# Performance work log

Hardware: AMD Instinct MI355X
Metric: run time of the kernel (lower is better)

The kernel has to match this reference:

```python
import jax, jax.numpy as jnp
import numpy as np

IMG_W, IMG_H, STRIDE = 640, 360, 32
S = 72
FMAP_H, FMAP_W = IMG_H // STRIDE, IMG_W // STRIDE  # 11, 20
C_IN, C_AF = 512, 64
B, T = 8, 4
LEFT = [72., 60., 49., 39., 30., 22.]
RIGHT = [108., 120., 131., 141., 150., 158.]
BOTTOM = [165., 150., 141., 131., 120., 108., 100., 90., 80., 72., 60., 49., 39., 30., 15.]


def _side_anchors(angles, nb, ys, x=None, y=None):
    # replicates LaneATT generate_side_anchors / generate_anchor, vectorized
    if x is not None:
        sx = np.full(nb, x, np.float64); sy = np.linspace(1., 0., nb)
    else:
        sx = np.linspace(1., 0., nb); sy = np.full(nb, y, np.float64)
    t = np.tan(np.deg2rad(np.asarray(angles, np.float64)))  # [J]
    # xs[i,j,s] = (sx_i + (1 - ys_s - 1 + sy_i)/tan(angle_j)) * img_w
    xs = (sx[:, None, None] + (1. - ys[None, None, :] - 1. + sy[:, None, None]) / t[None, :, None]) * IMG_W
    n = nb * len(angles)
    A = np.zeros((n, 5 + len(ys)), np.float32)
    A[:, 2] = np.repeat(1. - sy, len(angles))
    A[:, 3] = np.repeat(sx, len(angles))
    A[:, 5:] = xs.reshape(n, len(ys)).astype(np.float32)
    return A


def _gen_anchors(ys):
    left = _side_anchors(LEFT, 72, ys, x=0.)
    right = _side_anchors(RIGHT, 72, ys, x=1.)
    bottom = _side_anchors(BOTTOM, 128, ys, y=1.)
    return np.concatenate([left, bottom, right], axis=0)


def setup_inputs() -> dict:
    key = jax.random.key(0)
    ks = jax.random.split(key, 10)
    anchors = _gen_anchors(np.linspace(1., 0., S))            # [A, 77]
    anchors_cut = _gen_anchors(np.linspace(1., 0., FMAP_H))   # [A, 16]
    A = anchors.shape[0]  # 2784
    # compute_anchor_cut_indices
    unclamped = np.flip(np.round(anchors_cut[:, 5:] / STRIDE), axis=1).astype(np.int32)  # [A, H]
    cut_xs = np.clip(unclamped, 0, FMAP_W - 1)
    invalid_mask = (unclamped < 0) | (unclamped > FMAP_W)
    D = C_AF * FMAP_H  # 704
    head_in = (T + 1) * D  # (time_window_size+1)*anchor_feat_channels*fmap_h = 3520
    inp = {
        'x': jax.random.normal(ks[0], (B, T, C_IN, FMAP_H, FMAP_W), jnp.float32),
        'conv1_w': jax.random.normal(ks[1], (C_AF, C_IN), jnp.float32) * 0.02,
        'conv1_b': jnp.zeros((C_AF,), jnp.float32),
        'att_w': jax.random.normal(ks[2], (D, A - 1), jnp.float32) * 0.001,
        'att_b': jnp.zeros((A - 1,), jnp.float32),
        'cls_w': jax.random.normal(ks[3], (head_in, 2), jnp.float32) * 0.001,
        'cls_b': jnp.zeros((2,), jnp.float32),
        'reg_w': jax.random.normal(ks[4], (head_in, S + 2), jnp.float32) * 0.001,
        'reg_b': jnp.zeros((S + 2,), jnp.float32),
        'anchors': jnp.asarray(anchors),
        'cut_xs': jnp.asarray(cut_xs),
        'invalid_mask': jnp.asarray(invalid_mask),
    }
    return inp


def reference(x, conv1_w, conv1_b, att_w, att_b, cls_w, cls_b, reg_w, reg_b,
              anchors, cut_xs, invalid_mask):
    B_, T_, _, H, W = x.shape
    A = anchors.shape[0]
    # conv1: 1x1 conv over backbone features
    feats = jnp.einsum('btchw,oc->btohw', x, conv1_w) + conv1_b[None, None, :, None, None]
    # cut_anchor_features: gather rois[b,t,c,a,h] = feats[b,t,c,h,cut_xs[a,h]]
    Hy = jnp.broadcast_to(jnp.arange(H), cut_xs.shape)       # [A, H]
    rois = feats[:, :, :, Hy, cut_xs]                        # [B, T, C_af, A, H]
    rois = jnp.where(invalid_mask[None, None, None], 0.0, rois)
    rois = jnp.transpose(rois, (0, 1, 3, 2, 4))              # [B, T, A, C_af, H]
    C_af = rois.shape[3]
    D = C_af * H
    past = rois[:, :-1].reshape(B_, T_ - 1, A, D)            # [B, T-1, A, D]
    cur = rois[:, -1].reshape(B_, A, D)                      # [B, A, D]
    # attention_mechanism: softmax scores scattered into off-diagonal of [A, A]
    scores = cur.reshape(B_ * A, D) @ att_w + att_b          # [B*A, A-1]
    att = jax.nn.softmax(scores, axis=1).reshape(B_, A, A - 1)
    j = jnp.arange(A)
    i = j[:, None]
    # column j of row i maps to source index j - (j>i); diagonal is zero
    k = jnp.minimum(jnp.where(j[None, :] > i, j[None, :] - 1, j[None, :]), A - 2)
    Ibd = jnp.broadcast_to(i, (A, A))
    M = jnp.where(jnp.eye(A, dtype=bool)[None], 0.0, att[:, Ibd, k])  # [B, A, A]
    att_feat = jnp.einsum('bia,bad->bid', M, cur)            # [B, A, D]
    # head input: [past frames | attention features | current frame]
    past_p = jnp.transpose(past, (0, 2, 1, 3)).reshape(B_ * A, (T_ - 1) * D)
    head_in = jnp.concatenate([past_p, att_feat.reshape(B_ * A, D), cur.reshape(B_ * A, D)], axis=1)
    cls = (head_in @ cls_w + cls_b).reshape(B_, A, 2)
    reg = (head_in @ reg_w + reg_b).reshape(B_, A, -1)       # [B, A, n_offsets+2]
    base = jnp.broadcast_to(anchors[None], (B_, A, anchors.shape[1]))
    # reg_proposals: [:, :, :2]=cls ; [:, :, 2] from anchor ; [:, :, 3:] = anchor + reg
    reg_proposals = jnp.concatenate([cls, base[..., 2:3], base[..., 3:] + reg], axis=-1)
    return reg_proposals  # [B, A, 5 + n_offsets]
```

## Files before the change

### kernel.cpp

```cpp
#include <hip/hip_runtime.h>

#define BB 8
#define TT 4
#define CIN 512
#define CAF 64
#define HH 11
#define WW 20
#define PP 220
#define PPAD 256
#define AREAL 2784
#define AP 2816
#define DD 704
#define NH 80
#define NHP 128
#define KH 3520
#define NATT 2783

typedef __attribute__((ext_vector_type(8))) short bf16x8;
typedef __attribute__((ext_vector_type(4))) float floatx4;

__device__ __forceinline__ short f2bf(float f) {
  unsigned u = __float_as_uint(f);
  u += 0x7fffu + ((u >> 16) & 1u);
  return (short)(u >> 16);
}
__device__ __forceinline__ float bf2f(short s) {
  return __uint_as_float(((unsigned)(unsigned short)s) << 16);
}

__device__ __forceinline__ void gload_lds16(const void* g, void* l) {
  __builtin_amdgcn_global_load_lds(
      (const __attribute__((address_space(1))) void*)g,
      (__attribute__((address_space(3))) void*)l, 16, 0, 0);
}

__global__ __launch_bounds__(256)
void transpose_x_kernel(const float* __restrict__ x, short* __restrict__ xT)
{
  int bt = blockIdx.x;
  int c0 = blockIdx.y * 32;
  __shared__ float xs[32 * PP];
  int tid = threadIdx.x;
  const float* xp = x + ((long)bt * CIN + c0) * PP;
  for (int i = tid; i < 32 * PP; i += 256) xs[i] = xp[i];
  __syncthreads();
  short* op = xT + (long)bt * PPAD * CIN + c0;
  for (int j = tid; j < PPAD * 32; j += 256) {
    int p = j >> 5, cc = j & 31;
    short v = 0;
    if (p < PP) v = f2bf(xs[cc * PP + p]);
    op[(long)p * CIN + cc] = v;
  }
}

__global__ void prep_wbf_kernel(const float* __restrict__ w, short* __restrict__ wb)
{
  int idx = blockIdx.x * 256 + threadIdx.x;
  if (idx >= 128 * CIN) return;
  int n = idx >> 9, c = idx & 511;
  wb[idx] = (n < CAF) ? f2bf(w[(long)n * CIN + c]) : (short)0;
}

__global__ void prep_gidx_kernel(const int* __restrict__ cut_xs, const int* __restrict__ invalid,
                                 int* __restrict__ gidx)
{
  int idx = blockIdx.x * 256 + threadIdx.x;
  if (idx >= AREAL * HH) return;
  int hh = idx % HH;
  gidx[idx] = invalid[idx] ? -1 : (hh * WW + cut_xs[idx]) * 128;
}

__global__ __launch_bounds__(256)
void gather_cur_kernel(const short* __restrict__ fpo_base, const int* __restrict__ gidx,
                       short* __restrict__ curR)
{
  int g = blockIdx.y;
  int idx = blockIdx.x * 256 + threadIdx.x;
  int a = idx / 88;
  int ch = idx - a * 88;
  int d0 = ch * 8;
  bf16x8 v = {};
  if (a < AREAL) {
    const short* fp = fpo_base + ((long)g * TT + 3) * PPAD * 128;
    #pragma unroll
    for (int e = 0; e < 8; ++e) {
      int d = d0 + e;
      int o = d / 11;
      int hh = d - o * 11;
      int gi = gidx[a * 11 + hh];
      v[e] = (gi < 0) ? (short)0 : fp[gi + o];
    }
  }
  *(bf16x8*)(curR + ((long)g * AP + a) * DD + d0) = v;
}

__global__ __launch_bounds__(256)
void gather_past_kernel(const short* __restrict__ fpo_base, const int* __restrict__ gidx,
                        short* __restrict__ pastR)
{
  int ty = blockIdx.y;
  int g = ty / 3, t = ty - g * 3;
  int idx = blockIdx.x * 256 + threadIdx.x;
  int a = idx / 88;
  int ch = idx - a * 88;
  int d0 = ch * 8;
  bf16x8 v = {};
  if (a < AREAL) {
    const short* fp = fpo_base + ((long)g * TT + t) * PPAD * 128;
    #pragma unroll
    for (int e = 0; e < 8; ++e) {
      int d = d0 + e;
      int o = d / 11;
      int hh = d - o * 11;
      int gi = gidx[a * 11 + hh];
      v[e] = (gi < 0) ? (short)0 : fp[gi + o];
    }
  }
  *(bf16x8*)(pastR + ((long)ty * AP + a) * DD + d0) = v;
}

__global__ __launch_bounds__(256)
void prep_attw_kernel(const float* __restrict__ att_w, short* __restrict__ attwT)
{
  int n0 = blockIdx.x * 32;
  int d0 = blockIdx.y * 32;
  __shared__ float tile[32][33];
  int tid = threadIdx.x;
  for (int i = tid; i < 1024; i += 256) {
    int r = i >> 5, c = i & 31;
    int d = d0 + r, n = n0 + c;
    tile[r][c] = (d < DD && n < NATT) ? att_w[(long)d * NATT + n] : 0.f;
  }
  __syncthreads();
  for (int i = tid; i < 1024; i += 256) {
    int r = i >> 5, c = i & 31;
    attwT[(long)(n0 + r) * DD + d0 + c] = f2bf(tile[c][r]);
  }
}

__global__ void prep_headw_kernel(const float* __restrict__ cls_w, const float* __restrict__ reg_w,
                                  short* __restrict__ headwT)
{
  long idx = (long)blockIdx.x * 256 + threadIdx.x;
  if (idx >= (long)NHP * KH) return;
  int n = (int)(idx / KH), k = (int)(idx % KH);
  float v = 0.f;
  if (n < 2) v = cls_w[(long)k * 2 + n];
  else if (n < 76) v = reg_w[(long)k * 74 + (n - 2)];
  headwT[idx] = f2bf(v);
}

__global__ __launch_bounds__(512, 2)
void gemm256_nt_kernel(const short* __restrict__ A, long long aBatch, int lda,
                       const short* __restrict__ Bt, long long bBatch, int ldb,
                       short* __restrict__ C, long long cBatch, int ldc,
                       int K, const float* __restrict__ bias, int biasN)
{
  int gx = gridDim.x, gy = gridDim.y;
  int nwg = gx * gy * gridDim.z;
  int o = blockIdx.x + gx * (blockIdx.y + gy * blockIdx.z);
  int xcd = o & 7, pos = o >> 3;
  int q = nwg >> 3, r = nwg & 7;
  int nid = (xcd < r ? xcd * (q + 1) : r * (q + 1) + (xcd - r) * q) + pos;
  int bx = nid % gx; int tq = nid / gx; int by = tq % gy; int bz = tq / gy;

  A  += (long long)bz * aBatch;
  Bt += (long long)bz * bBatch;
  C  += (long long)bz * cBatch;
  int M0 = by * 256, N0 = bx * 256;

  __shared__ short lds_a[2 * 256 * 64];
  __shared__ short lds_b[2 * 256 * 64];

  int tid = threadIdx.x, lane = tid & 63, w = tid >> 6;
  int wr = w >> 2, wc = w & 3;

  floatx4 acc[8][4];
  #pragma unroll
  for (int m = 0; m < 8; ++m)
    #pragma unroll
    for (int n = 0; n < 4; ++n) acc[m][n] = floatx4{0.f, 0.f, 0.f, 0.f};

  int rl = tid >> 3, sl = tid & 7;
  int ssl = sl ^ (rl & 7);
  const short* aS = A  + (long)(M0 + rl) * lda + ssl * 8;
  const short* bS = Bt + (long)(N0 + rl) * ldb + ssl * 8;
  char* la0 = (char*)lds_a;
  char* lb0 = (char*)lds_b;
  int wub = (tid & ~63) * 16;

  auto stage = [&](int kt, int buf) {
    long ko = (long)kt * 64;
    #pragma unroll
    for (int c = 0; c < 4; ++c) {
      gload_lds16(aS + (long)c * 64 * lda + ko, la0 + buf * 32768 + c * 8192 + wub);
      gload_lds16(bS + (long)c * 64 * ldb + ko, lb0 + buf * 32768 + c * 8192 + wub);
    }
  };
  auto rdA = [&](int buf, int mf, int kk) -> bf16x8 {
    int row = wr * 128 + mf * 16 + (lane & 15);
    int phys = (kk * 4 + (lane >> 4)) ^ (lane & 7);
    return *(const bf16x8*)(la0 + buf * 32768 + row * 128 + phys * 16);
  };
  auto rdB = [&](int buf, int nf, int kk) -> bf16x8 {
    int row = wc * 64 + nf * 16 + (lane & 15);
    int phys = (kk * 4 + (lane >> 4)) ^ (lane & 7);
    return *(const bf16x8*)(lb0 + buf * 32768 + row * 128 + phys * 16);
  };

  int nt = K >> 6;
  stage(0, 0);
  stage(1, 1);
  asm volatile("s_waitcnt vmcnt(8)" ::: "memory");
  __builtin_amdgcn_sched_barrier(0);
  __builtin_amdgcn_s_barrier();
  __builtin_amdgcn_sched_barrier(0);

  for (int t = 0; t < nt; ++t) {
    int buf = t & 1;
    bf16x8 A0[2][4], A1[2][4], B0[2][2], B1[2][2];
    #pragma unroll
    for (int kk = 0; kk < 2; ++kk) {
      #pragma unroll
      for (int i = 0; i < 4; ++i) A0[kk][i] = rdA(buf, i, kk);
      #pragma unroll
      for (int j = 0; j < 2; ++j) B0[kk][j] = rdB(buf, j, kk);
    }
    __builtin_amdgcn_s_setprio(1);
    #pragma unroll
    for (int kk = 0; kk < 2; ++kk)
      #pragma unroll
      for (int i = 0; i < 4; ++i)
        #pragma unroll
        for (int j = 0; j < 2; ++j)
          acc[i][j] = __builtin_amdgcn_mfma_f32_16x16x32_bf16(A0[kk][i], B0[kk][j], acc[i][j], 0, 0, 0);
    __builtin_amdgcn_s_setprio(0);
    #pragma unroll
    for (int kk = 0; kk < 2; ++kk)
      #pragma unroll
      for (int j = 0; j < 2; ++j) B1[kk][j] = rdB(buf, 2 + j, kk);
    __builtin_amdgcn_s_setprio(1);
    #pragma unroll
    for (int kk = 0; kk < 2; ++kk)
      #pragma unroll
      for (int i = 0; i < 4; ++i)
        #pragma unroll
        for (int j = 0; j < 2; ++j)
          acc[i][2 + j] = __builtin_amdgcn_mfma_f32_16x16x32_bf16(A0[kk][i], B1[kk][j], acc[i][2 + j], 0, 0, 0);
    __builtin_amdgcn_s_setprio(0);
    #pragma unroll
    for (int kk = 0; kk < 2; ++kk)
      #pragma unroll
      for (int i = 0; i < 4; ++i) A1[kk][i] = rdA(buf, 4 + i, kk);
    __builtin_amdgcn_s_setprio(1);
    #pragma unroll
    for (int kk = 0; kk < 2; ++kk)
      #pragma unroll
      for (int i = 0; i < 4; ++i)
        #pragma unroll
        for (int j = 0; j < 2; ++j)
          acc[4 + i][2 + j] = __builtin_amdgcn_mfma_f32_16x16x32_bf16(A1[kk][i], B1[kk][j], acc[4 + i][2 + j], 0, 0, 0);
    __builtin_amdgcn_s_setprio(0);
    __builtin_amdgcn_sched_barrier(0);
    __builtin_amdgcn_s_barrier();
    __builtin_amdgcn_sched_barrier(0);
    if (t + 2 < nt) stage(t + 2, buf);
    __builtin_amdgcn_s_setprio(1);
    #pragma unroll
    for (int kk = 0; kk < 2; ++kk)
      #pragma unroll
      for (int i = 0; i < 4; ++i)
        #pragma unroll
        for (int j = 0; j < 2; ++j)
          acc[4 + i][j] = __builtin_amdgcn_mfma_f32_16x16x32_bf16(A1[kk][i], B0[kk][j], acc[4 + i][j], 0, 0, 0);
    __builtin_amdgcn_s_setprio(0);
    if (t + 2 < nt) {
      asm volatile("s_waitcnt vmcnt(8)" ::: "memory");
    } else {
      asm volatile("s_waitcnt vmcnt(0)" ::: "memory");
    }
    __builtin_amdgcn_sched_barrier(0);
    __builtin_amdgcn_s_barrier();
    __builtin_amdgcn_sched_barrier(0);
  }

  #pragma unroll
  for (int mf = 0; mf < 8; ++mf) {
    #pragma unroll
    for (int nf = 0; nf < 4; ++nf) {
      int col = N0 + wc * 64 + nf * 16 + (lane & 15);
      float bv = 0.f;
      if (bias) bv = (col < biasN) ? bias[col] : 0.f;
      #pragma unroll
      for (int rr = 0; rr < 4; ++rr) {
        int rowc = M0 + wr * 128 + mf * 16 + (lane >> 4) * 4 + rr;
        C[(long)rowc * ldc + col] = f2bf(acc[mf][nf][rr] + bv);
      }
    }
  }
}

template<int WITH_BIAS>
__global__ __launch_bounds__(256)
void gemm_nt_kernel(const short* __restrict__ A, long long aBatch, int lda,
                    const short* __restrict__ Bt, long long bBatch, int ldb,
                    short* __restrict__ C, long long cBatch, int ldc,
                    int K, const float* __restrict__ bias, int biasN)
{
  int gx = gridDim.x, gy = gridDim.y;
  int nwg = gx * gy * gridDim.z;
  int o = blockIdx.x + gx * (blockIdx.y + gy * blockIdx.z);
  int xcd = o & 7, pos = o >> 3;
  int q = nwg >> 3, r = nwg & 7;
  int nid = (xcd < r ? xcd * (q + 1) : r * (q + 1) + (xcd - r) * q) + pos;
  int bx = nid % gx; int t = nid / gx; int by = t % gy; int bz = t / gy;

  A  += (long long)bz * aBatch;
  Bt += (long long)bz * bBatch;
  C  += (long long)bz * cBatch;
  int m0 = by * 128;
  int n0 = bx * 128;

  __shared__ short lds_a[2 * 128 * 32];
  __shared__ short lds_b[2 * 128 * 32];

  int tid = threadIdx.x;
  int lane = tid & 63;
  int wid = tid >> 6;
  int wr = wid >> 1, wc = wid & 1;
  int row = tid >> 2;
  int slot = tid & 3;

  floatx4 acc[4][4];
  #pragma unroll
  for (int m = 0; m < 4; ++m)
    #pragma unroll
    for (int n = 0; n < 4; ++n) acc[m][n] = floatx4{0.f, 0.f, 0.f, 0.f};

  int wbase = (tid & ~63) * 16;
  int ks0 = slot ^ ((row >> 1) & 3);
  int ks1 = slot ^ (((row + 64) >> 1) & 3);
  const short* ar0 = A  + (long)(m0 + row) * lda + ks0 * 8;
  const short* ar1 = A  + (long)(m0 + row + 64) * lda + ks1 * 8;
  const short* br0 = Bt + (long)(n0 + row) * ldb + ks0 * 8;
  const short* br1 = Bt + (long)(n0 + row + 64) * ldb + ks1 * 8;

  auto stage = [&](int kt, int buf) {
    int k0 = kt * 32;
    char* la = (char*)lds_a + buf * 8192 + wbase;
    char* lb = (char*)lds_b + buf * 8192 + wbase;
    gload_lds16(ar0 + k0, la);
    gload_lds16(ar1 + k0, la + 4096);
    gload_lds16(br0 + k0, lb);
    gload_lds16(br1 + k0, lb + 4096);
  };

  int nk = K >> 5;
  stage(0, 0);
  __syncthreads();
  int cur = 0;
  for (int kt = 0; kt < nk; ++kt) {
    if (kt + 1 < nk) stage(kt + 1, cur ^ 1);
    const char* ba = (const char*)lds_a + cur * 8192;
    const char* bb = (const char*)lds_b + cur * 8192;
    bf16x8 af[4], bfv[4];
    #pragma unroll
    for (int m = 0; m < 4; ++m) {
      int rw = wr * 64 + m * 16 + (lane & 15);
      int pp = (lane >> 4) ^ ((rw >> 1) & 3);
      af[m] = *(const bf16x8*)(ba + rw * 64 + (pp << 4));
    }
    #pragma unroll
    for (int n = 0; n < 4; ++n) {
      int rw = wc * 64 + n * 16 + (lane & 15);
      int pp = (lane >> 4) ^ ((rw >> 1) & 3);
      bfv[n] = *(const bf16x8*)(bb + rw * 64 + (pp << 4));
    }
    #pragma unroll
    for (int m = 0; m < 4; ++m)
      #pragma unroll
      for (int n = 0; n < 4; ++n)
        acc[m][n] = __builtin_amdgcn_mfma_f32_16x16x32_bf16(af[m], bfv[n], acc[m][n], 0, 0, 0);
    __syncthreads();
    cur ^= 1;
  }

  #pragma unroll
  for (int m = 0; m < 4; ++m) {
    #pragma unroll
    for (int n = 0; n < 4; ++n) {
      int col = n0 + wc * 64 + n * 16 + (lane & 15);
      float bv = 0.f;
      if (WITH_BIAS) bv = (col < biasN) ? bias[col] : 0.f;
      #pragma unroll
      for (int rr = 0; rr < 4; ++rr) {
        int rowc = m0 + wr * 64 + m * 16 + (lane >> 4) * 4 + rr;
        C[(long)rowc * ldc + col] = f2bf(acc[m][n][rr] + bv);
      }
    }
  }
}

__global__ __launch_bounds__(256)
void softmax_shift_kernel(short* __restrict__ scores)
{
  int g = blockIdx.y;
  int i = blockIdx.x;
  short* row = scores + (long)g * AP * AP + (long)i * AP;
  __shared__ float vals[NATT];
  __shared__ float red[4];
  int tid = threadIdx.x;

  float lmax = -1e30f;
  for (int jc = tid; jc < 348; jc += 256) {
    bf16x8 v8 = *(const bf16x8*)(row + jc * 8);
    #pragma unroll
    for (int e = 0; e < 8; ++e) {
      int j = jc * 8 + e;
      float f = bf2f(v8[e]);
      if (j < NATT) { vals[j] = f; lmax = fmaxf(lmax, f); }
    }
  }
  #pragma unroll
  for (int off = 32; off; off >>= 1) lmax = fmaxf(lmax, __shfl_down(lmax, off, 64));
  if ((tid & 63) == 0) red[tid >> 6] = lmax;
  __syncthreads();
  float mx = fmaxf(fmaxf(red[0], red[1]), fmaxf(red[2], red[3]));
  __syncthreads();

  float lsum = 0.f;
  for (int j = tid; j < NATT; j += 256) {
    float e = __expf(vals[j] - mx);
    vals[j] = e;
    lsum += e;
  }
  #pragma unroll
  for (int off = 32; off; off >>= 1) lsum += __shfl_down(lsum, off, 64);
  if ((tid & 63) == 0) red[tid >> 6] = lsum;
  __syncthreads();
  float inv = 1.f / (red[0] + red[1] + red[2] + red[3]);
  __syncthreads();

  for (int jc = tid; jc < 352; jc += 256) {
    bf16x8 o8;
    #pragma unroll
    for (int e = 0; e < 8; ++e) {
      int j = jc * 8 + e;
      float v;
      if (j < i)            v = vals[j] * inv;
      else if (j == i)      v = 0.f;
      else if (j < AREAL)   v = vals[j - 1] * inv;
      else                  v = 0.f;
      o8[e] = f2bf(v);
    }
    *(bf16x8*)(row + jc * 8) = o8;
  }
}

__device__ __forceinline__
void gemm_n80_body(const short* __restrict__ abase, int ald, int m0,
                   const short* __restrict__ hb, int ldbh,
                   short* __restrict__ lp, int nk,
                   short* lds_a, short* lds_b)
{
  int tid = threadIdx.x, lane = tid & 63, wid = tid >> 6;

  floatx4 acc[2][5];
  #pragma unroll
  for (int m = 0; m < 2; ++m)
    #pragma unroll
    for (int n = 0; n < 5; ++n) acc[m][n] = floatx4{0.f, 0.f, 0.f, 0.f};

  int wbase = (tid & ~63) * 16;
  int row = tid >> 2;
  int slot = tid & 3;
  int ks0 = slot ^ ((row >> 1) & 3);
  int ks1 = slot ^ (((row + 64) >> 1) & 3);
  const short* ar0 = abase + (long)(m0 + row) * ald + ks0 * 8;
  const short* ar1 = abase + (long)(m0 + row + 64) * ald + ks1 * 8;
  const short* br0 = hb + (long)row * ldbh + ks0 * 8;
  const short* br1 = hb + (long)(row + 64) * ldbh + ks1 * 8;

  auto stage = [&](int kt, int buf) {
    int k0 = kt * 32;
    char* la = (char*)lds_a + buf * 8192 + wbase;
    char* lb = (char*)lds_b + buf * 8192 + wbase;
    gload_lds16(ar0 + k0, la);
    gload_lds16(ar1 + k0, la + 4096);
    gload_lds16(br0 + k0, lb);
    gload_lds16(br1 + k0, lb + 4096);
  };

  stage(0, 0);
  __syncthreads();
  int cur = 0;
  for (int kt = 0; kt < nk; ++kt) {
    if (kt + 1 < nk) stage(kt + 1, cur ^ 1);
    const char* la = (const char*)lds_a + cur * 8192;
    const char* lb = (const char*)lds_b + cur * 8192;
    bf16x8 af[2], bfv[5];
    #pragma unroll
    for (int m = 0; m < 2; ++m) {
      int rw = wid * 32 + m * 16 + (lane & 15);
      int pp = (lane >> 4) ^ ((rw >> 1) & 3);
      af[m] = *(const bf16x8*)(la + rw * 64 + (pp << 4));
    }
    #pragma unroll
    for (int n = 0; n < 5; ++n) {
      int nn = n * 16 + (lane & 15);
      int pp = (lane >> 4) ^ ((nn >> 1) & 3);
      bfv[n] = *(const bf16x8*)(lb + nn * 64 + (pp << 4));
    }
    #pragma unroll
    for (int m = 0; m < 2; ++m)
      #pragma unroll
      for (int n = 0; n < 5; ++n)
        acc[m][n] = __builtin_amdgcn_mfma_f32_16x16x32_bf16(af[m], bfv[n], acc[m][n], 0, 0, 0);
    __syncthreads();
    cur ^= 1;
  }

  #pragma unroll
  for (int fm = 0; fm < 2; ++fm)
    #pragma unroll
    for (int fn = 0; fn < 5; ++fn)
      #pragma unroll
      for (int rr = 0; rr < 4; ++rr) {
        int rw = m0 + wid * 32 + fm * 16 + (lane >> 4) * 4 + rr;
        int col = fn * 16 + (lane & 15);
        lp[(long)rw * NH + col] = f2bf(acc[fm][fn][rr]);
      }
}

__global__ __launch_bounds__(256)
void gemm_heads_kernel(const short* __restrict__ pastR, const short* __restrict__ curR,
                       const short* __restrict__ headwT, short* __restrict__ linpart, int G)
{
  int kc = blockIdx.x;
  int m0 = blockIdx.y * 128;
  int g  = blockIdx.z;
  const short* abase;
  const short* hb;
  if (kc == 3) { abase = curR + (long)g * AP * DD; hb = headwT + 4 * DD; }
  else         { abase = pastR + (long)(g * 3 + kc) * AP * DD; hb = headwT + kc * DD; }
  __shared__ short lds_a[2 * 128 * 32];
  __shared__ short lds_b[2 * 128 * 32];
  short* lp = linpart + (long)(kc * G + g) * AP * NH;
  gemm_n80_body(abase, DD, m0, hb, KH, lp, DD / 32, lds_a, lds_b);
}

__global__ __launch_bounds__(256)
void gemm_skinny_kernel(const short* __restrict__ scores, const short* __restrict__ curW3T,
                        short* __restrict__ linpart, int G)
{
  int kc = blockIdx.x;
  int m0 = blockIdx.y * 128;
  int g  = blockIdx.z;
  const short* abase = scores + (long)g * AP * AP + (long)kc * 704;
  const short* hb    = curW3T + (long)g * NHP * AP + (long)kc * 704;
  __shared__ short lds_a[2 * 128 * 32];
  __shared__ short lds_b[2 * 128 * 32];
  short* lp = linpart + (long)((4 + kc) * G + g) * AP * NH;
  gemm_n80_body(abase, AP, m0, hb, AP, lp, 704 / 32, lds_a, lds_b);
}

__global__ void assemble_kernel(const short* __restrict__ linpart, const float* __restrict__ anchors,
                                const float* __restrict__ cls_b, const float* __restrict__ reg_b,
                                float* __restrict__ out_b0, int G)
{
  long idx = (long)blockIdx.x * 256 + threadIdx.x;
  const long per_g = (long)AREAL * 77;
  if (idx >= per_g * G) return;
  int g = (int)(idx / per_g);
  long rem = idx - (long)g * per_g;
  int c = (int)(rem % 77);
  int a = (int)(rem / 77);
  float v;
  if (c == 2) {
    v = anchors[(long)a * 77 + 2];
  } else {
    int col = (c < 2) ? c : (2 + (c - 3));
    float s = 0.f;
    #pragma unroll
    for (int sl = 0; sl < 8; ++sl)
      s += bf2f(linpart[((long)(sl * G + g) * AP + a) * NH + col]);
    v = (c < 2) ? (s + cls_b[c]) : (anchors[(long)a * 77 + c] + s + reg_b[c - 3]);
  }
  out_b0[idx] = v;
}

extern "C" void kernel_launch(void* const* d_in, const int* in_sizes, int n_in,
                              void* d_out, int out_size, void* d_ws, size_t ws_size,
                              hipStream_t stream)
{
  (void)in_sizes; (void)n_in; (void)out_size;
  const float* x        = (const float*)d_in[0];
  const float* conv1_w  = (const float*)d_in[1];
  const float* conv1_b  = (const float*)d_in[2];
  const float* att_w    = (const float*)d_in[3];
  const float* att_b    = (const float*)d_in[4];
  const float* cls_w    = (const float*)d_in[5];
  const float* cls_b    = (const float*)d_in[6];
  const float* reg_w    = (const float*)d_in[7];
  const float* reg_b    = (const float*)d_in[8];
  const float* anchors  = (const float*)d_in[9];
  const int*   cut_xs   = (const int*)d_in[10];
  const int*   invalid  = (const int*)d_in[11];
  float* out = (float*)d_out;

  auto align256 = [](size_t v) { return (v + 255) & ~(size_t)255; };
  const size_t sz_feats  = align256((size_t)BB * TT * PPAD * 128 * 2);
  const size_t sz_wbf    = align256((size_t)128 * CIN * 2);
  const size_t sz_attwT  = align256((size_t)AP * DD * 2);
  const size_t sz_headwT = align256((size_t)NHP * KH * 2);
  const size_t sz_gidx   = align256((size_t)AREAL * HH * 4);
  const size_t misc = sz_feats + sz_wbf + sz_attwT + sz_headwT + sz_gidx;
  auto per_g = [&](int G) {
    return align256((size_t)G * AP * DD * 2)
         + align256((size_t)G * AP * AP * 2)
         + align256((size_t)G * NHP * AP * 2)
         + align256((size_t)8 * G * AP * NH * 2);
  };
  int G = 1;
  for (int cand : {8, 4, 2}) {
    if (misc + per_g(cand) + (1u << 20) <= ws_size) { G = cand; break; }
  }

  char* p = (char*)d_ws;
  short* feats_po = (short*)p; p += sz_feats;
  short* w_bf16   = (short*)p; p += sz_wbf;
  short* attwT    = (short*)p; p += sz_attwT;
  short* headwT   = (short*)p; p += sz_headwT;
  int*   gidx     = (int*)p;   p += sz_gidx;
  short* curR     = (short*)p; p += align256((size_t)G * AP * DD * 2);
  short* scores   = (short*)p; p += align256((size_t)G * AP * AP * 2);
  short* curW3T   = (short*)p; p += align256((size_t)G * NHP * AP * 2);
  short* linpart  = (short*)p; p += align256((size_t)8 * G * AP * NH * 2);
  short* xT       = scores;
  short* pastR    = scores;

  transpose_x_kernel<<<dim3(BB * TT, CIN / 32), 256, 0, stream>>>(x, xT);
  prep_wbf_kernel<<<(128 * CIN + 255) / 256, 256, 0, stream>>>(conv1_w, w_bf16);
  prep_attw_kernel<<<dim3(AP / 32, DD / 32), 256, 0, stream>>>(att_w, attwT);
  prep_headw_kernel<<<(NHP * KH + 255) / 256, 256, 0, stream>>>(cls_w, reg_w, headwT);
  prep_gidx_kernel<<<(AREAL * HH + 255) / 256, 256, 0, stream>>>(cut_xs, invalid, gidx);

  gemm_nt_kernel<1><<<dim3(1, BB * TT * PPAD / 128, 1), 256, 0, stream>>>(
      xT, 0, CIN, w_bf16, 0, CIN, feats_po, 0, 128, CIN, conv1_b, CAF);

  for (int b0 = 0; b0 < BB; b0 += G) {
    const short* fpo = feats_po + (long)b0 * TT * PPAD * 128;

    gather_cur_kernel<<<dim3(AP * 88 / 256, G), 256, 0, stream>>>(fpo, gidx, curR);

    gemm256_nt_kernel<<<dim3(AP / 256, G * AP / 256, 1), 512, 0, stream>>>(
        curR, 0, DD, attwT, 0, DD, scores, 0, AP, DD, att_b, NATT);

    softmax_shift_kernel<<<dim3(AREAL, G), 256, 0, stream>>>(scores);

    gemm_nt_kernel<0><<<dim3(AP / 128, 1, G), 256, 0, stream>>>(
        headwT + 3 * DD, 0, KH, curR, (long long)AP * DD, DD,
        curW3T, (long long)NHP * AP, AP, DD, nullptr, 0);

    gemm_skinny_kernel<<<dim3(4, AP / 128, G), 256, 0, stream>>>(scores, curW3T, linpart, G);

    gather_past_kernel<<<dim3(AP * 88 / 256, 3 * G), 256, 0, stream>>>(fpo, gidx, pastR);

    gemm_heads_kernel<<<dim3(4, AP / 128, G), 256, 0, stream>>>(pastR, curR, headwT, linpart, G);

    assemble_kernel<<<(int)(((long)G * AREAL * 77 + 255) / 256), 256, 0, stream>>>(
        linpart, anchors, cls_b, reg_b, out + (long)b0 * AREAL * 77, G);
  }
}
```

Measured before the change: 379.6 us.

## Replace head GEMMs with precomputed per-position projection tables and gathers

```diff
diff --git a/kernel.cpp b/kernel.cpp
--- a/kernel.cpp
+++ b/kernel.cpp
@@ -13,7 +13,6 @@
 #define DD 704
 #define NH 80
 #define NHP 128
-#define KH 3520
 #define NATT 2783
 
 typedef __attribute__((ext_vector_type(8))) short bf16x8;
@@ -95,31 +94,6 @@
 }
 
 __global__ __launch_bounds__(256)
-void gather_past_kernel(const short* __restrict__ fpo_base, const int* __restrict__ gidx,
-                        short* __restrict__ pastR)
-{
-  int ty = blockIdx.y;
-  int g = ty / 3, t = ty - g * 3;
-  int idx = blockIdx.x * 256 + threadIdx.x;
-  int a = idx / 88;
-  int ch = idx - a * 88;
-  int d0 = ch * 8;
-  bf16x8 v = {};
-  if (a < AREAL) {
-    const short* fp = fpo_base + ((long)g * TT + t) * PPAD * 128;
-    #pragma unroll
-    for (int e = 0; e < 8; ++e) {
-      int d = d0 + e;
-      int o = d / 11;
-      int hh = d - o * 11;
-      int gi = gidx[a * 11 + hh];
-      v[e] = (gi < 0) ? (short)0 : fp[gi + o];
-    }
-  }
-  *(bf16x8*)(pastR + ((long)ty * AP + a) * DD + d0) = v;
-}
-
-__global__ __launch_bounds__(256)
 void prep_attw_kernel(const float* __restrict__ att_w, short* __restrict__ attwT)
 {
   int n0 = blockIdx.x * 32;
@@ -138,16 +112,85 @@
   }
 }
 
-__global__ void prep_headw_kernel(const float* __restrict__ cls_w, const float* __restrict__ reg_w,
-                                  short* __restrict__ headwT)
-{
-  long idx = (long)blockIdx.x * 256 + threadIdx.x;
-  if (idx >= (long)NHP * KH) return;
-  int n = (int)(idx / KH), k = (int)(idx % KH);
-  float v = 0.f;
-  if (n < 2) v = cls_w[(long)k * 2 + n];
-  else if (n < 76) v = reg_w[(long)k * 74 + (n - 2)];
-  headwT[idx] = f2bf(v);
+__global__ __launch_bounds__(256)
+void prep_tables_kernel(const short* __restrict__ feats_po,
+                        const float* __restrict__ cls_w, const float* __restrict__ reg_w,
+                        float* __restrict__ T)
+{
+  int bid = blockIdx.x;
+  int b = bid / 55; int r = bid - b * 55; int t5 = r / 11; int hh = r - t5 * 11;
+  int tsel = t5 < 3 ? t5 : 3;
+  const short* fp = feats_po + ((long)(b * TT + tsel) * PPAD + hh * WW) * 128;
+  __shared__ float fs[20 * 64];
+  __shared__ float wsl[80 * 65];
+  int tid = threadIdx.x;
+  for (int i = tid; i < 1280; i += 256) {
+    int x = i >> 6, o = i & 63;
+    fs[i] = bf2f(fp[x * 128 + o]);
+  }
+  for (int i = tid; i < 5120; i += 256) {
+    int n = i >> 6, o = i & 63;
+    int k = t5 * DD + o * 11 + hh;
+    float v = 0.f;
+    if (n < 2) v = cls_w[(long)k * 2 + n];
+    else if (n < 76) v = reg_w[(long)k * 74 + (n - 2)];
+    wsl[n * 65 + o] = v;
+  }
+  __syncthreads();
+  float* Tb = T + (long)bid * 1600;
+  for (int j = tid; j < 1600; j += 256) {
+    int x = j / 80, n = j - (j / 80) * 80;
+    float s = 0.f;
+    #pragma unroll
+    for (int o = 0; o < 64; ++o) s += fs[x * 64 + o] * wsl[n * 65 + o];
+    Tb[x * 80 + n] = s;
+  }
+}
+
+__global__ __launch_bounds__(256)
+void tgather_heads_kernel(const float* __restrict__ T, const int* __restrict__ cut_xs,
+                          const int* __restrict__ invalid, short* __restrict__ linpart,
+                          int b0, int G)
+{
+  int g = blockIdx.y; int b = b0 + g;
+  int idx = blockIdx.x * 256 + threadIdx.x;
+  if (idx >= AREAL * 80) return;
+  int a = idx / 80, n = idx - (idx / 80) * 80;
+  const float* Tb = T + (long)b * 55 * 1600;
+  float s = 0.f;
+  #pragma unroll
+  for (int hh = 0; hh < 11; ++hh) {
+    int x = cut_xs[a * 11 + hh];
+    if (!invalid[a * 11 + hh]) {
+      int base = x * 80 + n;
+      s += Tb[(0 * 11 + hh) * 1600 + base];
+      s += Tb[(1 * 11 + hh) * 1600 + base];
+      s += Tb[(2 * 11 + hh) * 1600 + base];
+      s += Tb[(4 * 11 + hh) * 1600 + base];
+    }
+  }
+  linpart[((long)(0 * G + g) * AP + a) * NH + n] = f2bf(s);
+}
+
+__global__ __launch_bounds__(256)
+void tgather_w3_kernel(const float* __restrict__ T, const int* __restrict__ cut_xs,
+                       const int* __restrict__ invalid, short* __restrict__ curW3T,
+                       int b0, int G)
+{
+  int g = blockIdx.y; int b = b0 + g;
+  int idx = blockIdx.x * 256 + threadIdx.x;
+  if (idx >= NHP * AP) return;
+  int n = idx / AP, j = idx - (idx / AP) * AP;
+  float s = 0.f;
+  if (n < 80 && j < AREAL) {
+    const float* Tb = T + ((long)b * 55 + 3 * 11) * 1600;
+    #pragma unroll
+    for (int hh = 0; hh < 11; ++hh) {
+      int x = cut_xs[j * 11 + hh];
+      if (!invalid[j * 11 + hh]) s += Tb[hh * 1600 + x * 80 + n];
+    }
+  }
+  curW3T[(long)g * NHP * AP + idx] = f2bf(s);
 }
 
 __global__ __launch_bounds__(512, 2)
@@ -533,23 +576,6 @@
 }
 
 __global__ __launch_bounds__(256)
-void gemm_heads_kernel(const short* __restrict__ pastR, const short* __restrict__ curR,
-                       const short* __restrict__ headwT, short* __restrict__ linpart, int G)
-{
-  int kc = blockIdx.x;
-  int m0 = blockIdx.y * 128;
-  int g  = blockIdx.z;
-  const short* abase;
-  const short* hb;
-  if (kc == 3) { abase = curR + (long)g * AP * DD; hb = headwT + 4 * DD; }
-  else         { abase = pastR + (long)(g * 3 + kc) * AP * DD; hb = headwT + kc * DD; }
-  __shared__ short lds_a[2 * 128 * 32];
-  __shared__ short lds_b[2 * 128 * 32];
-  short* lp = linpart + (long)(kc * G + g) * AP * NH;
-  gemm_n80_body(abase, DD, m0, hb, KH, lp, DD / 32, lds_a, lds_b);
-}
-
-__global__ __launch_bounds__(256)
 void gemm_skinny_kernel(const short* __restrict__ scores, const short* __restrict__ curW3T,
                         short* __restrict__ linpart, int G)
 {
@@ -560,7 +586,7 @@
   const short* hb    = curW3T + (long)g * NHP * AP + (long)kc * 704;
   __shared__ short lds_a[2 * 128 * 32];
   __shared__ short lds_b[2 * 128 * 32];
-  short* lp = linpart + (long)((4 + kc) * G + g) * AP * NH;
+  short* lp = linpart + (long)((1 + kc) * G + g) * AP * NH;
   gemm_n80_body(abase, AP, m0, hb, AP, lp, 704 / 32, lds_a, lds_b);
 }
 
@@ -582,7 +608,7 @@
     int col = (c < 2) ? c : (2 + (c - 3));
     float s = 0.f;
     #pragma unroll
-    for (int sl = 0; sl < 8; ++sl)
+    for (int sl = 0; sl < 5; ++sl)
       s += bf2f(linpart[((long)(sl * G + g) * AP + a) * NH + col]);
     v = (c < 2) ? (s + cls_b[c]) : (anchors[(long)a * 77 + c] + s + reg_b[c - 3]);
   }
@@ -612,14 +638,14 @@
   const size_t sz_feats  = align256((size_t)BB * TT * PPAD * 128 * 2);
   const size_t sz_wbf    = align256((size_t)128 * CIN * 2);
   const size_t sz_attwT  = align256((size_t)AP * DD * 2);
-  const size_t sz_headwT = align256((size_t)NHP * KH * 2);
   const size_t sz_gidx   = align256((size_t)AREAL * HH * 4);
-  const size_t misc = sz_feats + sz_wbf + sz_attwT + sz_headwT + sz_gidx;
+  const size_t sz_T      = align256((size_t)BB * 55 * 1600 * 4);
+  const size_t misc = sz_feats + sz_wbf + sz_attwT + sz_gidx + sz_T;
   auto per_g = [&](int G) {
     return align256((size_t)G * AP * DD * 2)
          + align256((size_t)G * AP * AP * 2)
          + align256((size_t)G * NHP * AP * 2)
-         + align256((size_t)8 * G * AP * NH * 2);
+         + align256((size_t)5 * G * AP * NH * 2);
   };
   int G = 1;
   for (int cand : {8, 4, 2}) {
@@ -630,43 +656,41 @@
   short* feats_po = (short*)p; p += sz_feats;
   short* w_bf16   = (short*)p; p += sz_wbf;
   short* attwT    = (short*)p; p += sz_attwT;
-  short* headwT   = (short*)p; p += sz_headwT;
   int*   gidx     = (int*)p;   p += sz_gidx;
+  float* T        = (float*)p; p += sz_T;
   short* curR     = (short*)p; p += align256((size_t)G * AP * DD * 2);
   short* scores   = (short*)p; p += align256((size_t)G * AP * AP * 2);
   short* curW3T   = (short*)p; p += align256((size_t)G * NHP * AP * 2);
-  short* linpart  = (short*)p; p += align256((size_t)8 * G * AP * NH * 2);
+  short* linpart  = (short*)p; p += align256((size_t)5 * G * AP * NH * 2);
   short* xT       = scores;
-  short* pastR    = scores;
 
   transpose_x_kernel<<<dim3(BB * TT, CIN / 32), 256, 0, stream>>>(x, xT);
   prep_wbf_kernel<<<(128 * CIN + 255) / 256, 256, 0, stream>>>(conv1_w, w_bf16);
   prep_attw_kernel<<<dim3(AP / 32, DD / 32), 256, 0, stream>>>(att_w, attwT);
-  prep_headw_kernel<<<(NHP * KH + 255) / 256, 256, 0, stream>>>(cls_w, reg_w, headwT);
   prep_gidx_kernel<<<(AREAL * HH + 255) / 256, 256, 0, stream>>>(cut_xs, invalid, gidx);
 
   gemm_nt_kernel<1><<<dim3(1, BB * TT * PPAD / 128, 1), 256, 0, stream>>>(
       xT, 0, CIN, w_bf16, 0, CIN, feats_po, 0, 128, CIN, conv1_b, CAF);
 
+  prep_tables_kernel<<<BB * 55, 256, 0, stream>>>(feats_po, cls_w, reg_w, T);
+
   for (int b0 = 0; b0 < BB; b0 += G) {
     const short* fpo = feats_po + (long)b0 * TT * PPAD * 128;
 
     gather_cur_kernel<<<dim3(AP * 88 / 256, G), 256, 0, stream>>>(fpo, gidx, curR);
 
+    tgather_w3_kernel<<<dim3((NHP * AP + 255) / 256, G), 256, 0, stream>>>(
+        T, cut_xs, invalid, curW3T, b0, G);
+
+    tgather_heads_kernel<<<dim3((AREAL * 80 + 255) / 256, G), 256, 0, stream>>>(
+        T, cut_xs, invalid, linpart, b0, G);
+
     gemm256_nt_kernel<<<dim3(AP / 256, G * AP / 256, 1), 512, 0, stream>>>(
         curR, 0, DD, attwT, 0, DD, scores, 0, AP, DD, att_b, NATT);
 
     softmax_shift_kernel<<<dim3(AREAL, G), 256, 0, stream>>>(scores);
 
-    gemm_nt_kernel<0><<<dim3(AP / 128, 1, G), 256, 0, stream>>>(
-        headwT + 3 * DD, 0, KH, curR, (long long)AP * DD, DD,
-        curW3T, (long long)NHP * AP, AP, DD, nullptr, 0);
-
     gemm_skinny_kernel<<<dim3(4, AP / 128, G), 256, 0, stream>>>(scores, curW3T, linpart, G);
-
-    gather_past_kernel<<<dim3(AP * 88 / 256, 3 * G), 256, 0, stream>>>(fpo, gidx, pastR);
-
-    gemm_heads_kernel<<<dim3(4, AP / 128, G), 256, 0, stream>>>(pastR, curR, headwT, linpart, G);
 
     assemble_kernel<<<(int)(((long)G * AREAL * 77 + 255) / 256), 256, 0, stream>>>(
         linpart, anchors, cls_b, reg_b, out + (long)b0 * AREAL * 77, G);
```

New measurement: 359.2 us (median of 2 runs). 1.06x faster.
